# Kernel tuning notes

Measured on AMD Instinct MI355X. Metric: run time of the kernel, lower is better.

The kernel has to match this reference:

```python
import jax, jax.numpy as jnp
import numpy as np

T, B, I, H, LBL = 200, 1024, 128, 128, 4


def setup_inputs() -> dict:
    key = jax.random.key(0)
    ks = jax.random.split(key, 14)
    si = 1.0 / np.sqrt(I)
    sh = 1.0 / np.sqrt(H)
    inputs = jax.random.normal(ks[0], (T, B, I), jnp.float32)
    lengths = jnp.maximum(jax.random.randint(ks[1], (B,), 1, T + 1), LBL).astype(jnp.int32)
    return {
        "inputs": inputs,
        "lengths": lengths,
        "Wih_g": jax.random.normal(ks[2], (3 * H, I), jnp.float32) * si,
        "Whh_g": jax.random.normal(ks[3], (3 * H, H), jnp.float32) * sh,
        "bih_g": jax.random.normal(ks[4], (3 * H,), jnp.float32) * sh,
        "bhh_g": jax.random.normal(ks[5], (3 * H,), jnp.float32) * sh,
        "Wih_l": jax.random.normal(ks[6], (3 * H, I), jnp.float32) * si,
        "Whh_l": jax.random.normal(ks[7], (3 * H, H), jnp.float32) * sh,
        "bih_l": jax.random.normal(ks[8], (3 * H,), jnp.float32) * sh,
        "bhh_l": jax.random.normal(ks[9], (3 * H,), jnp.float32) * sh,
        "A1": jax.random.normal(ks[10], (H, H), jnp.float32) * sh,
        "A2": jax.random.normal(ks[11], (H, H), jnp.float32) * sh,
        "v1": jax.random.normal(ks[12], (1, H), jnp.float32) * sh,
        "label_len": LBL,
    }


def gru(x, Wih, Whh, bih, bhh):
    # x: [T, B, I] time-major. PyTorch GRU cell semantics.
    Bq, Hq = x.shape[1], Whh.shape[1]
    gi_all = jnp.einsum('tbi,gi->tbg', x, Wih) + bih  # precompute input projections [T,B,3H]
    def step(h, gi):
        gh = h @ Whh.T + bhh
        ir, iz, inn = jnp.split(gi, 3, axis=-1)
        hr, hz, hn = jnp.split(gh, 3, axis=-1)
        r = jax.nn.sigmoid(ir + hr)
        z = jax.nn.sigmoid(iz + hz)
        n = jnp.tanh(inn + r * hn)
        h = (1.0 - z) * n + z * h
        return h, h
    h0 = jnp.zeros((Bq, Hq), x.dtype)
    _, hs = jax.lax.scan(step, h0, gi_all)
    return hs  # [T, B, H]


def reference(inputs, lengths, Wih_g, Whh_g, bih_g, bhh_g,
              Wih_l, Whh_l, bih_l, bhh_l, A1, A2, v1, label_len):
    h_g = gru(inputs, Wih_g, Whh_g, bih_g, bhh_g)  # [T,B,H]
    h_l = gru(inputs, Wih_l, Whh_l, bih_l, bhh_l)  # [T,B,H]
    # attention score per step s: v1(sigmoid(A1 h_l + A2 h_g)), query-independent
    pre = jax.nn.sigmoid(jnp.einsum('tbh,gh->tbg', h_l, A1) +
                         jnp.einsum('tbh,gh->tbg', h_g, A2))
    scores = jnp.einsum('tbg,og->tbo', pre, v1)  # [T,B,1]
    # per-t output = cumsum_{s<=t}(score*h_l) + h_g[t]
    out = jnp.cumsum(scores * h_l, axis=0) + h_g  # [T,B,H]
    out_b = jnp.transpose(out, (1, 0, 2))  # [B,T,H]
    # gather last label_len timesteps of each sequence: h[b,k] = out[L_b-label_len+k, b]
    idx = lengths[:, None].astype(jnp.int32) - label_len + jnp.arange(label_len, dtype=jnp.int32)[None, :]
    idx = jnp.clip(idx, 0, out_b.shape[1] - 1)  # [B, label_len]
    h = jnp.take_along_axis(out_b, idx[:, :, None], axis=1)  # [B, label_len, H]
    return h
```

## Files before the change

kernel.cpp:

```cpp
#include <hip/hip_runtime.h>
#include <stdint.h>


typedef __attribute__((ext_vector_type(8))) short short8;
typedef __attribute__((ext_vector_type(4))) float float4v;

__device__ inline float bf2f(unsigned short u){
  union { unsigned int i; float f; } v; v.i = ((unsigned int)u) << 16; return v.f;
}
__device__ inline unsigned short f2bf(float f){
  union { float f; unsigned int i; } v; v.f = f;
  unsigned int x = v.i;
  return (unsigned short)((x + 0x7fffu + ((x >> 16) & 1u)) >> 16);
}
__device__ inline unsigned int pack2(float a, float b){
  return (unsigned int)f2bf(a) | ((unsigned int)f2bf(b) << 16);
}
__device__ inline float sigm(float x){ return __builtin_amdgcn_rcpf(1.0f + __expf(-x)); }
__device__ inline float tanhfast(float x){ return 1.0f - 2.0f * __builtin_amdgcn_rcpf(__expf(2.0f * x) + 1.0f); }

__global__ void k_prep(unsigned short* hl_slot, unsigned short* hg_slot, float* cum)
{
  int i = blockIdx.x * blockDim.x + threadIdx.x;
  hl_slot[i] = 0;
  hg_slot[i] = 0;
  cum[i] = 0.0f;
}

__global__ __launch_bounds__(512, 2) void k_scan(
    const float* __restrict__ x,
    const float* __restrict__ Wih_g, const float* __restrict__ Whh_g,
    const float* __restrict__ bih_g, const float* __restrict__ bhh_g,
    const float* __restrict__ Wih_l, const float* __restrict__ Whh_l,
    const float* __restrict__ bih_l, const float* __restrict__ bhh_l,
    unsigned short* __restrict__ hl_seq, unsigned short* __restrict__ hg_seq,
    int tc, int t0)
{
  __shared__ __align__(16) unsigned short hbuf[2][16][136];
  __shared__ __align__(16) unsigned short xbuf[2][16][136];
  int tid = threadIdx.x;
  int w = tid >> 6, L = tid & 63, l15 = L & 15, q = L >> 4;
  int gru = blockIdx.x & 1;
  int b0 = (blockIdx.x >> 1) * 16;
  const float* Wih = gru ? Wih_l : Wih_g;
  const float* Whh = gru ? Whh_l : Whh_g;
  const float* bih = gru ? bih_l : bih_g;
  const float* bhh = gru ? bhh_l : bhh_g;
  unsigned short* myseq = gru ? hl_seq : hg_seq;

  int col = w * 16 + l15;

  short8 Wi[3][4], Wh[3][4];
  #pragma unroll
  for (int G = 0; G < 3; G++) {
    int row = G * 128 + col;
    #pragma unroll
    for (int kf = 0; kf < 4; kf++) {
      const float4* p0 = (const float4*)(Wih + (size_t)row * 128 + kf * 32 + q * 8);
      const float4* p1 = (const float4*)(Whh + (size_t)row * 128 + kf * 32 + q * 8);
      float4 a0 = p0[0], a1 = p0[1], b0f = p1[0], b1f = p1[1];
      short8 si, sh;
      si[0]=(short)f2bf(a0.x); si[1]=(short)f2bf(a0.y); si[2]=(short)f2bf(a0.z); si[3]=(short)f2bf(a0.w);
      si[4]=(short)f2bf(a1.x); si[5]=(short)f2bf(a1.y); si[6]=(short)f2bf(a1.z); si[7]=(short)f2bf(a1.w);
      sh[0]=(short)f2bf(b0f.x); sh[1]=(short)f2bf(b0f.y); sh[2]=(short)f2bf(b0f.z); sh[3]=(short)f2bf(b0f.w);
      sh[4]=(short)f2bf(b1f.x); sh[5]=(short)f2bf(b1f.y); sh[6]=(short)f2bf(b1f.z); sh[7]=(short)f2bf(b1f.w);
      Wi[G][kf] = si; Wh[G][kf] = sh;
    }
  }
  float br  = bih[col]       + bhh[col];
  float bz  = bih[128 + col] + bhh[128 + col];
  float bin = bih[256 + col];
  float bnh = bhh[256 + col];

  float hold[4];
  #pragma unroll
  for (int r = 0; r < 4; r++) {
    int m = q * 4 + r;
    unsigned short u = myseq[((size_t)(tc - 1) * 1024 + b0 + m) * 128 + col];
    hold[r] = bf2f(u);
    hbuf[0][m][col] = u;
  }
  {
    float4 x0 = ((const float4*)(x + ((size_t)t0 * 1024 + b0) * 128))[tid];
    int row = tid >> 5, c4 = (tid & 31) * 4;
    *(uint2*)&xbuf[0][row][c4] = make_uint2(pack2(x0.x, x0.y), pack2(x0.z, x0.w));
  }
  int tn = t0 + (tc > 1 ? 1 : 0);
  float4 xr = ((const float4*)(x + ((size_t)tn * 1024 + b0) * 128))[tid];
  __syncthreads();

  int p = 0;
  for (int s = 0; s < tc; s++) {
    short8 Ah[4], Ax[4];
    #pragma unroll
    for (int kf = 0; kf < 4; kf++) {
      Ah[kf] = *(const short8*)&hbuf[p][l15][kf * 32 + q * 8];
      Ax[kf] = *(const short8*)&xbuf[p][l15][kf * 32 + q * 8];
    }
    if (s + 1 < tc) {
      int row = tid >> 5, c4 = (tid & 31) * 4;
      *(uint2*)&xbuf[1 - p][row][c4] = make_uint2(pack2(xr.x, xr.y), pack2(xr.z, xr.w));
    }
    {
      int t2 = t0 + (s + 2 < tc ? s + 2 : tc - 1);
      xr = ((const float4*)(x + ((size_t)t2 * 1024 + b0) * 128))[tid];
    }
    float4v arz0 = (float4v){0.f,0.f,0.f,0.f};
    float4v arz1 = (float4v){0.f,0.f,0.f,0.f};
    float4v anx  = (float4v){0.f,0.f,0.f,0.f};
    float4v anh  = (float4v){0.f,0.f,0.f,0.f};
    #pragma unroll
    for (int kf = 0; kf < 4; kf++) arz0 = __builtin_amdgcn_mfma_f32_16x16x32_bf16(Ax[kf], Wi[0][kf], arz0, 0,0,0);
    #pragma unroll
    for (int kf = 0; kf < 4; kf++) arz0 = __builtin_amdgcn_mfma_f32_16x16x32_bf16(Ah[kf], Wh[0][kf], arz0, 0,0,0);
    #pragma unroll
    for (int kf = 0; kf < 4; kf++) arz1 = __builtin_amdgcn_mfma_f32_16x16x32_bf16(Ax[kf], Wi[1][kf], arz1, 0,0,0);
    #pragma unroll
    for (int kf = 0; kf < 4; kf++) arz1 = __builtin_amdgcn_mfma_f32_16x16x32_bf16(Ah[kf], Wh[1][kf], arz1, 0,0,0);
    #pragma unroll
    for (int kf = 0; kf < 4; kf++) anx  = __builtin_amdgcn_mfma_f32_16x16x32_bf16(Ax[kf], Wi[2][kf], anx,  0,0,0);
    #pragma unroll
    for (int kf = 0; kf < 4; kf++) anh  = __builtin_amdgcn_mfma_f32_16x16x32_bf16(Ah[kf], Wh[2][kf], anh,  0,0,0);

    #pragma unroll
    for (int r = 0; r < 4; r++) {
      int m = q * 4 + r;
      float rr = sigm(arz0[r] + br);
      float zz = sigm(arz1[r] + bz);
      float nn = tanhfast(anx[r] + bin + rr * (anh[r] + bnh));
      float hn = nn + zz * (hold[r] - nn);
      hold[r] = hn;
      unsigned short hu = f2bf(hn);
      hbuf[1 - p][m][col] = hu;
      myseq[((size_t)s * 1024 + b0 + m) * 128 + col] = hu;
    }
    p ^= 1;
    __syncthreads();
  }
}

__global__ __launch_bounds__(256) void k_score(const unsigned short* __restrict__ hl_seq,
                                               const unsigned short* __restrict__ hg_seq,
                                               const float* __restrict__ A1,
                                               const float* __restrict__ A2,
                                               const float* __restrict__ v1,
                                               float* __restrict__ score, int tc)
{
  __shared__ __align__(16) unsigned short Mt[128][136];
  int tid = threadIdx.x;
  int w = tid >> 6, L = tid & 63;
  int l15 = L & 15, q = L >> 4;
  int tile = blockIdx.x * 4 + w;
  int s = tile >> 6;
  int b0 = (tile & 63) * 16;

  short8 Fl[4], Fg[4];
  #pragma unroll
  for (int kf = 0; kf < 4; kf++) {
    size_t base = ((size_t)s * 1024 + b0 + l15) * 128 + kf * 32 + q * 8;
    Fl[kf] = *(const short8*)(hl_seq + base);
    Fg[kf] = *(const short8*)(hg_seq + base);
  }
  float4v acc[8];
  #pragma unroll
  for (int nt = 0; nt < 8; nt++) acc[nt] = (float4v){0.f, 0.f, 0.f, 0.f};

  #pragma unroll
  for (int it = 0; it < 16; it++) {
    int f4 = it * 256 + tid;
    float4 a = ((const float4*)A1)[f4];
    *(uint2*)&Mt[f4 >> 5][(f4 & 31) * 4] = make_uint2(pack2(a.x, a.y), pack2(a.z, a.w));
  }
  __syncthreads();
  #pragma unroll
  for (int nt = 0; nt < 8; nt++)
    #pragma unroll
    for (int kf = 0; kf < 4; kf++)
      acc[nt] = __builtin_amdgcn_mfma_f32_16x16x32_bf16(
          Fl[kf], *(const short8*)&Mt[nt * 16 + l15][kf * 32 + q * 8], acc[nt], 0, 0, 0);
  __syncthreads();
  #pragma unroll
  for (int it = 0; it < 16; it++) {
    int f4 = it * 256 + tid;
    float4 a = ((const float4*)A2)[f4];
    *(uint2*)&Mt[f4 >> 5][(f4 & 31) * 4] = make_uint2(pack2(a.x, a.y), pack2(a.z, a.w));
  }
  __syncthreads();
  #pragma unroll
  for (int nt = 0; nt < 8; nt++)
    #pragma unroll
    for (int kf = 0; kf < 4; kf++)
      acc[nt] = __builtin_amdgcn_mfma_f32_16x16x32_bf16(
          Fg[kf], *(const short8*)&Mt[nt * 16 + l15][kf * 32 + q * 8], acc[nt], 0, 0, 0);

  float v1v[8];
  #pragma unroll
  for (int nt = 0; nt < 8; nt++) v1v[nt] = v1[nt * 16 + l15];

  float p4[4];
  #pragma unroll
  for (int r = 0; r < 4; r++) {
    float sum = 0.f;
    #pragma unroll
    for (int nt = 0; nt < 8; nt++) sum += v1v[nt] * sigm(acc[nt][r]);
    sum += __shfl_xor(sum, 1, 16);
    sum += __shfl_xor(sum, 2, 16);
    sum += __shfl_xor(sum, 4, 16);
    sum += __shfl_xor(sum, 8, 16);
    p4[r] = sum;
  }
  if (l15 == 0) {
    #pragma unroll
    for (int r = 0; r < 4; r++)
      score[(size_t)(b0 + q * 4 + r) * tc + s] = p4[r];
  }
}

__global__ __launch_bounds__(256) void k_cum(const float* __restrict__ score,
                                             const unsigned short* __restrict__ hl_seq,
                                             const unsigned short* __restrict__ hg_seq,
                                             const int* __restrict__ lengths,
                                             float* __restrict__ cum,
                                             float* __restrict__ out, int tc, int t0)
{
  __shared__ __align__(16) unsigned short hlL[100 * 256];
  __shared__ float scL[2][100];
  int tid = threadIdx.x;
  int b2 = tid >> 7, j = tid & 127;
  int b0 = blockIdx.x * 2;
  int b = b0 + b2;
  int base = b2 * 128 + j;

  float c = cum[(size_t)b * 128 + j];
  int cap0 = lengths[b] - 4;

  float hgv[4];
  #pragma unroll
  for (int d = 0; d < 4; d++) {
    int sl = cap0 + d - t0;
    hgv[d] = (sl >= 0 && sl < tc) ? bf2f(hg_seq[((size_t)sl * 1024 + b) * 128 + j]) : 0.f;
  }

  for (int seg = 0; seg < tc; seg += 100) {
    int len = (tc - seg < 100) ? (tc - seg) : 100;
    __syncthreads();
    for (int f8 = tid; f8 < len * 32; f8 += 256) {
      int sl = f8 >> 5, r8 = f8 & 31;
      *(short8*)&hlL[(size_t)f8 * 8] =
          *(const short8*)(hl_seq + ((size_t)(seg + sl) * 1024 + b0) * 128 + r8 * 8);
    }
    for (int i = tid; i < 2 * len; i += 256) {
      int bb = (i >= len) ? 1 : 0;
      int sl = i - bb * len;
      scL[bb][sl] = score[(size_t)(b0 + bb) * tc + seg + sl];
    }
    __syncthreads();

    int sl = 0;
    for (; sl + 5 <= len; sl += 5) {
      float h[5], sc[5];
      #pragma unroll
      for (int k = 0; k < 5; k++) {
        h[k] = bf2f(hlL[(size_t)(sl + k) * 256 + base]);
        sc[k] = scL[b2][sl + k];
      }
      #pragma unroll
      for (int k = 0; k < 5; k++) {
        c += sc[k] * h[k];
        int d = (t0 + seg + sl + k) - cap0;
        if ((unsigned)d < 4u)
          out[((size_t)b * 4 + d) * 128 + j] = c + hgv[d];
      }
    }
    for (; sl < len; sl++) {
      c += scL[b2][sl] * bf2f(hlL[(size_t)sl * 256 + base]);
      int d = (t0 + seg + sl) - cap0;
      if ((unsigned)d < 4u)
        out[((size_t)b * 4 + d) * 128 + j] = c + hgv[d];
    }
  }
  cum[(size_t)b * 128 + j] = c;
}

extern "C" void kernel_launch(void* const* d_in, const int* in_sizes, int n_in,
                              void* d_out, int out_size, void* d_ws, size_t ws_size,
                              hipStream_t stream)
{
  const float* x     = (const float*)d_in[0];
  const int* lengths = (const int*)d_in[1];
  const float* Wih_g = (const float*)d_in[2];
  const float* Whh_g = (const float*)d_in[3];
  const float* bih_g = (const float*)d_in[4];
  const float* bhh_g = (const float*)d_in[5];
  const float* Wih_l = (const float*)d_in[6];
  const float* Whh_l = (const float*)d_in[7];
  const float* bih_l = (const float*)d_in[8];
  const float* bhh_l = (const float*)d_in[9];
  const float* A1    = (const float*)d_in[10];
  const float* A2    = (const float*)d_in[11];
  const float* v1    = (const float*)d_in[12];
  float* out = (float*)d_out;

  const int cands[8] = {200, 100, 50, 25, 10, 5, 2, 1};
  int tc = 0;
  for (int i = 0; i < 8; i++) {
    int T = cands[i];
    size_t need = 2 * (size_t)T * 1024 * 128 * 2
                + (size_t)T * 1024 * 4
                + 524288;
    if (need <= ws_size) { tc = T; break; }
  }
  if (!tc) return;

  char* wsb = (char*)d_ws;
  size_t o = 0;
  unsigned short* hl  = (unsigned short*)(wsb + o); o += (size_t)tc * 1024 * 128 * 2;
  unsigned short* hg  = (unsigned short*)(wsb + o); o += (size_t)tc * 1024 * 128 * 2;
  float* score = (float*)(wsb + o); o += (size_t)tc * 1024 * 4;
  float* cum   = (float*)(wsb + o);

  unsigned short* hl_slot = hl + (size_t)(tc - 1) * 1024 * 128;
  unsigned short* hg_slot = hg + (size_t)(tc - 1) * 1024 * 128;

  k_prep<<<512, 256, 0, stream>>>(hl_slot, hg_slot, cum);
  int nch = 200 / tc;
  for (int c = 0; c < nch; c++) {
    k_scan<<<128, 512, 0, stream>>>(x, Wih_g, Whh_g, bih_g, bhh_g,
                                    Wih_l, Whh_l, bih_l, bhh_l, hl, hg, tc, c * tc);
    k_score<<<tc * 16, 256, 0, stream>>>(hl, hg, A1, A2, v1, score, tc);
    k_cum<<<512, 256, 0, stream>>>(score, hl, hg, lengths, cum, out, tc, c * tc);
  }
}
```

Baseline: 426.5 us.

## Amortize attention weight staging across batch tiles and reorder scan MFMAs

The score kernel now launches one block per timestep. Each block converts A1 and A2 to bf16 in LDS once and loops over all 64 batch tiles, prefetching the next tile's hidden states into registers, instead of restaging both matrices for every 4 tiles. In the recurrent scan, the input-projection MFMAs are issued before the hidden-state ones, and __syncthreads is replaced by an LDS-only waitcnt plus s_barrier. The change trades grid parallelism in the score kernel for less redundant weight traffic, and it relies on the custom barrier being sufficient for the scan's global stores.

```diff
diff --git a/kernel.cpp b/kernel.cpp
--- a/kernel.cpp
+++ b/kernel.cpp
@@ -4,6 +4,8 @@
 
 typedef __attribute__((ext_vector_type(8))) short short8;
 typedef __attribute__((ext_vector_type(4))) float float4v;
+
+#define LDS_BARRIER() asm volatile("s_waitcnt lgkmcnt(0)\n\ts_barrier" ::: "memory")
 
 __device__ inline float bf2f(unsigned short u){
   union { unsigned int i; float f; } v; v.i = ((unsigned int)u) << 16; return v.f;
@@ -112,15 +114,15 @@
     #pragma unroll
     for (int kf = 0; kf < 4; kf++) arz0 = __builtin_amdgcn_mfma_f32_16x16x32_bf16(Ax[kf], Wi[0][kf], arz0, 0,0,0);
     #pragma unroll
+    for (int kf = 0; kf < 4; kf++) arz1 = __builtin_amdgcn_mfma_f32_16x16x32_bf16(Ax[kf], Wi[1][kf], arz1, 0,0,0);
+    #pragma unroll
+    for (int kf = 0; kf < 4; kf++) anx  = __builtin_amdgcn_mfma_f32_16x16x32_bf16(Ax[kf], Wi[2][kf], anx,  0,0,0);
+    #pragma unroll
+    for (int kf = 0; kf < 4; kf++) anh  = __builtin_amdgcn_mfma_f32_16x16x32_bf16(Ah[kf], Wh[2][kf], anh,  0,0,0);
+    #pragma unroll
     for (int kf = 0; kf < 4; kf++) arz0 = __builtin_amdgcn_mfma_f32_16x16x32_bf16(Ah[kf], Wh[0][kf], arz0, 0,0,0);
     #pragma unroll
-    for (int kf = 0; kf < 4; kf++) arz1 = __builtin_amdgcn_mfma_f32_16x16x32_bf16(Ax[kf], Wi[1][kf], arz1, 0,0,0);
-    #pragma unroll
     for (int kf = 0; kf < 4; kf++) arz1 = __builtin_amdgcn_mfma_f32_16x16x32_bf16(Ah[kf], Wh[1][kf], arz1, 0,0,0);
-    #pragma unroll
-    for (int kf = 0; kf < 4; kf++) anx  = __builtin_amdgcn_mfma_f32_16x16x32_bf16(Ax[kf], Wi[2][kf], anx,  0,0,0);
-    #pragma unroll
-    for (int kf = 0; kf < 4; kf++) anh  = __builtin_amdgcn_mfma_f32_16x16x32_bf16(Ah[kf], Wh[2][kf], anh,  0,0,0);
 
     #pragma unroll
     for (int r = 0; r < 4; r++) {
@@ -135,7 +137,7 @@
       myseq[((size_t)s * 1024 + b0 + m) * 128 + col] = hu;
     }
     p ^= 1;
-    __syncthreads();
+    LDS_BARRIER();
   }
 }
 
@@ -146,73 +148,79 @@
                                                const float* __restrict__ v1,
                                                float* __restrict__ score, int tc)
 {
-  __shared__ __align__(16) unsigned short Mt[128][136];
+  __shared__ __align__(16) unsigned short M1[128][136];
+  __shared__ __align__(16) unsigned short M2[128][136];
   int tid = threadIdx.x;
   int w = tid >> 6, L = tid & 63;
   int l15 = L & 15, q = L >> 4;
-  int tile = blockIdx.x * 4 + w;
-  int s = tile >> 6;
-  int b0 = (tile & 63) * 16;
-
-  short8 Fl[4], Fg[4];
-  #pragma unroll
-  for (int kf = 0; kf < 4; kf++) {
-    size_t base = ((size_t)s * 1024 + b0 + l15) * 128 + kf * 32 + q * 8;
-    Fl[kf] = *(const short8*)(hl_seq + base);
-    Fg[kf] = *(const short8*)(hg_seq + base);
-  }
-  float4v acc[8];
-  #pragma unroll
-  for (int nt = 0; nt < 8; nt++) acc[nt] = (float4v){0.f, 0.f, 0.f, 0.f};
+  int s = blockIdx.x;
 
   #pragma unroll
   for (int it = 0; it < 16; it++) {
     int f4 = it * 256 + tid;
     float4 a = ((const float4*)A1)[f4];
-    *(uint2*)&Mt[f4 >> 5][(f4 & 31) * 4] = make_uint2(pack2(a.x, a.y), pack2(a.z, a.w));
+    float4 b = ((const float4*)A2)[f4];
+    *(uint2*)&M1[f4 >> 5][(f4 & 31) * 4] = make_uint2(pack2(a.x, a.y), pack2(a.z, a.w));
+    *(uint2*)&M2[f4 >> 5][(f4 & 31) * 4] = make_uint2(pack2(b.x, b.y), pack2(b.z, b.w));
   }
   __syncthreads();
-  #pragma unroll
-  for (int nt = 0; nt < 8; nt++)
-    #pragma unroll
-    for (int kf = 0; kf < 4; kf++)
-      acc[nt] = __builtin_amdgcn_mfma_f32_16x16x32_bf16(
-          Fl[kf], *(const short8*)&Mt[nt * 16 + l15][kf * 32 + q * 8], acc[nt], 0, 0, 0);
-  __syncthreads();
-  #pragma unroll
+
+  float v1v[8];
+  #pragma unroll
+  for (int nt = 0; nt < 8; nt++) v1v[nt] = v1[nt * 16 + l15];
+
+  short8 Fl[4], Fg[4], Pl[4], Pg[4];
+  {
+    size_t base = ((size_t)s * 1024 + (size_t)w * 16 + l15) * 128;
+    #pragma unroll
+    for (int kf = 0; kf < 4; kf++) {
+      Fl[kf] = *(const short8*)(hl_seq + base + kf * 32 + q * 8);
+      Fg[kf] = *(const short8*)(hg_seq + base + kf * 32 + q * 8);
+    }
+  }
   for (int it = 0; it < 16; it++) {
-    int f4 = it * 256 + tid;
-    float4 a = ((const float4*)A2)[f4];
-    *(uint2*)&Mt[f4 >> 5][(f4 & 31) * 4] = make_uint2(pack2(a.x, a.y), pack2(a.z, a.w));
-  }
-  __syncthreads();
-  #pragma unroll
-  for (int nt = 0; nt < 8; nt++)
-    #pragma unroll
-    for (int kf = 0; kf < 4; kf++)
-      acc[nt] = __builtin_amdgcn_mfma_f32_16x16x32_bf16(
-          Fg[kf], *(const short8*)&Mt[nt * 16 + l15][kf * 32 + q * 8], acc[nt], 0, 0, 0);
-
-  float v1v[8];
-  #pragma unroll
-  for (int nt = 0; nt < 8; nt++) v1v[nt] = v1[nt * 16 + l15];
-
-  float p4[4];
-  #pragma unroll
-  for (int r = 0; r < 4; r++) {
-    float sum = 0.f;
-    #pragma unroll
-    for (int nt = 0; nt < 8; nt++) sum += v1v[nt] * sigm(acc[nt][r]);
-    sum += __shfl_xor(sum, 1, 16);
-    sum += __shfl_xor(sum, 2, 16);
-    sum += __shfl_xor(sum, 4, 16);
-    sum += __shfl_xor(sum, 8, 16);
-    p4[r] = sum;
-  }
-  if (l15 == 0) {
-    #pragma unroll
-    for (int r = 0; r < 4; r++)
-      score[(size_t)(b0 + q * 4 + r) * tc + s] = p4[r];
+    int b0 = (it * 4 + w) * 16;
+    if (it + 1 < 16) {
+      size_t base = ((size_t)s * 1024 + (size_t)((it + 1) * 4 + w) * 16 + l15) * 128;
+      #pragma unroll
+      for (int kf = 0; kf < 4; kf++) {
+        Pl[kf] = *(const short8*)(hl_seq + base + kf * 32 + q * 8);
+        Pg[kf] = *(const short8*)(hg_seq + base + kf * 32 + q * 8);
+      }
+    }
+    float4v acc[8];
+    #pragma unroll
+    for (int nt = 0; nt < 8; nt++) {
+      float4v a = (float4v){0.f, 0.f, 0.f, 0.f};
+      #pragma unroll
+      for (int kf = 0; kf < 4; kf++)
+        a = __builtin_amdgcn_mfma_f32_16x16x32_bf16(
+            Fl[kf], *(const short8*)&M1[nt * 16 + l15][kf * 32 + q * 8], a, 0, 0, 0);
+      #pragma unroll
+      for (int kf = 0; kf < 4; kf++)
+        a = __builtin_amdgcn_mfma_f32_16x16x32_bf16(
+            Fg[kf], *(const short8*)&M2[nt * 16 + l15][kf * 32 + q * 8], a, 0, 0, 0);
+      acc[nt] = a;
+    }
+    float p4[4];
+    #pragma unroll
+    for (int r = 0; r < 4; r++) {
+      float sum = 0.f;
+      #pragma unroll
+      for (int nt = 0; nt < 8; nt++) sum += v1v[nt] * sigm(acc[nt][r]);
+      sum += __shfl_xor(sum, 1, 16);
+      sum += __shfl_xor(sum, 2, 16);
+      sum += __shfl_xor(sum, 4, 16);
+      sum += __shfl_xor(sum, 8, 16);
+      p4[r] = sum;
+    }
+    if (l15 == 0) {
+      #pragma unroll
+      for (int r = 0; r < 4; r++)
+        score[(size_t)(b0 + q * 4 + r) * tc + s] = p4[r];
+    }
+    #pragma unroll
+    for (int kf = 0; kf < 4; kf++) { Fl[kf] = Pl[kf]; Fg[kf] = Pg[kf]; }
   }
 }
 
@@ -327,7 +335,7 @@
   for (int c = 0; c < nch; c++) {
     k_scan<<<128, 512, 0, stream>>>(x, Wih_g, Whh_g, bih_g, bhh_g,
                                     Wih_l, Whh_l, bih_l, bhh_l, hl, hg, tc, c * tc);
-    k_score<<<tc * 16, 256, 0, stream>>>(hl, hg, A1, A2, v1, score, tc);
+    k_score<<<tc, 256, 0, stream>>>(hl, hg, A1, A2, v1, score, tc);
     k_cum<<<512, 256, 0, stream>>>(score, hl, hg, lengths, cum, out, tc, c * tc);
   }
 }
```

Result: slower. 438.1 us (+2.7%).
